# Kernel optimization log

Measured on AMD Instinct MI355X. Metric: run time of the kernel, lower is better.

The kernel has to match this reference:

```python
import jax, jax.numpy as jnp
import numpy as np

EPS = 1e-12

def l2norm(x):
    return x / jnp.maximum(jnp.linalg.norm(x, axis=-1, keepdims=True), EPS)

def setup_inputs() -> dict:
    key = jax.random.key(0)
    ks = jax.random.split(key, 10)
    B, N, Din, D, P, C = 2, 32768, 768, 512, 16, 2
    return {
        "x_s": jax.random.normal(ks[0], (B, N, Din), jnp.float32),
        "coord_s": jax.random.uniform(ks[1], (B, N, 2), jnp.float32),
        "x_l": jax.random.normal(ks[2], (B, N, Din), jnp.float32),
        "coord_l": jax.random.uniform(ks[3], (B, N, 2), jnp.float32),
        "W_proj": jax.random.normal(ks[4], (Din, D), jnp.float32) / np.sqrt(Din),
        "b_proj": jax.random.normal(ks[5], (D,), jnp.float32) * 0.01,
        "prototypes": jax.random.normal(ks[6], (P, D), jnp.float32),
        "text_low": l2norm(jax.random.normal(ks[7], (C, D), jnp.float32)),
        "text_high": l2norm(jax.random.normal(ks[8], (C, D), jnp.float32)),
        "label": jax.random.randint(ks[9], (B,), 0, C, jnp.int64),
    }

def forward_project(x, W, b):
    # Linear projection to hidden size, then L2 normalize (matches visual.forward_project + F.normalize)
    return l2norm(jnp.einsum('bni,id->bnd', x, W) + b)

def attention_pool(feats, prototypes):
    # feats: [B,N,D], prototypes: [P,D]
    D = feats.shape[-1]
    p = l2norm(prototypes)
    scores = jnp.einsum('bnd,pd->bpn', feats, p) / jnp.sqrt(jnp.asarray(D, feats.dtype))
    w = jax.nn.softmax(scores, axis=-1)                  # [B,P,N]
    attended = jnp.einsum('bpn,bnd->bpd', w, feats)       # [B,P,D]
    return l2norm(attended.mean(axis=1))                  # [B,D]

def reference(x_s, coord_s, x_l, coord_l, W_proj, b_proj, prototypes, text_low, text_high, label):
    x_s_proj = forward_project(x_s, W_proj, b_proj)
    x_l_proj = forward_project(x_l, W_proj, b_proj)
    feat_low = attention_pool(x_s_proj, prototypes)
    feat_high = attention_pool(x_l_proj, prototypes)
    logits = feat_low @ text_low.T + feat_high @ text_high.T   # [B,C]
    logp = jax.nn.log_softmax(logits, axis=-1)
    loss = -jnp.mean(jnp.take_along_axis(logp, label[:, None], axis=1))
    Y_prob = jax.nn.softmax(logits, axis=1)
    Y_hat = jnp.argmax(Y_prob, axis=1)
    return Y_prob, Y_hat, loss
```

## Files before the change

### kernel.cpp

```cpp
#include <hip/hip_runtime.h>
#include <math.h>

#define BB   2
#define NN   32768
#define DIN  768
#define DD   512
#define PP   16
#define MTOT (BB*NN)
#define MALL (2*MTOT)
#define NCHUNK 128
#define CHUNK  (NN/NCHUNK)
#define SCALE_INV_SQRT_D 0.04419417382415922f

typedef unsigned short u16;
typedef __attribute__((ext_vector_type(8))) short bf16x8;
typedef __attribute__((ext_vector_type(4))) float f32x4;

#define MFMA(a,b,c) __builtin_amdgcn_mfma_f32_16x16x32_bf16((a),(b),(c),0,0,0)

__device__ __forceinline__ unsigned pack2bf(float a, float b) {
  union { float f; unsigned u; } x{a}, y{b};
  unsigned ra = (x.u + 0x7FFFu + ((x.u >> 16) & 1u)) >> 16;
  unsigned rb = (y.u + 0x7FFFu + ((y.u >> 16) & 1u)) >> 16;
  return ra | (rb << 16);
}
__device__ __forceinline__ u16 f2bf(float a) {
  union { float f; unsigned u; } x{a};
  return (u16)((x.u + 0x7FFFu + ((x.u >> 16) & 1u)) >> 16);
}
__device__ __forceinline__ float bf2f(u16 u) {
  union { unsigned u; float f; } x; x.u = ((unsigned)u) << 16; return x.f;
}

__device__ __forceinline__ float block_reduce_sum_256(float v, float* sred) {
  #pragma unroll
  for (int off = 32; off; off >>= 1) v += __shfl_down(v, off);
  const int lane = threadIdx.x & 63, w = threadIdx.x >> 6;
  if (lane == 0) sred[w] = v;
  __syncthreads();
  float r = sred[0] + sred[1] + sred[2] + sred[3];
  __syncthreads();
  return r;
}

__global__ __launch_bounds__(64) void pre_kernel(
    const float* __restrict__ W, const float* __restrict__ prot,
    uint4* __restrict__ Bf, uint4* __restrict__ pnb) {
  const int bid = blockIdx.x;
  const int lane = threadIdx.x;
  if (bid < 768) {
    const int nf = bid / 24, ks = bid % 24;
    const int n = nf*16 + (lane & 15);
    const int kb = ks*32 + (lane >> 4)*8;
    unsigned r0 = pack2bf(W[(size_t)(kb+0)*DD + n], W[(size_t)(kb+1)*DD + n]);
    unsigned r1 = pack2bf(W[(size_t)(kb+2)*DD + n], W[(size_t)(kb+3)*DD + n]);
    unsigned r2 = pack2bf(W[(size_t)(kb+4)*DD + n], W[(size_t)(kb+5)*DD + n]);
    unsigned r3 = pack2bf(W[(size_t)(kb+6)*DD + n], W[(size_t)(kb+7)*DD + n]);
    Bf[(size_t)bid*64 + lane] = make_uint4(r0, r1, r2, r3);
    return;
  }
  const int ks = bid - 768;
  const int p = lane & 15, seg = lane >> 4;
  float ssq = 0.f;
  for (int d = seg*128; d < seg*128 + 128; d += 4) {
    float4 v = *(const float4*)&prot[p*DD + d];
    ssq += v.x*v.x + v.y*v.y + v.z*v.z + v.w*v.w;
  }
  ssq += __shfl_xor(ssq, 16);
  ssq += __shfl_xor(ssq, 32);
  const float rnp = 1.f / fmaxf(sqrtf(ssq), 1e-12f);
  const int kb = ks*32 + seg*8;
  float v[8];
  #pragma unroll
  for (int j = 0; j < 8; ++j) v[j] = prot[p*DD + kb + j] * rnp;
  pnb[ks*64 + lane] = make_uint4(pack2bf(v[0],v[1]), pack2bf(v[2],v[3]),
                                 pack2bf(v[4],v[5]), pack2bf(v[6],v[7]));
}

__global__ __launch_bounds__(512, 4) void gemm_kernel(
    const float* __restrict__ Xs, const float* __restrict__ Xl,
    const uint4* __restrict__ Bf, const float* __restrict__ bias,
    u16* __restrict__ proj, float* __restrict__ rnormb) {
  __shared__ __align__(16) unsigned char lds[73728];
  const int t = threadIdx.x, lane = t & 63, wn = t >> 6;
  const int cl = lane & 15, cg = lane >> 4;
  const int m0g = blockIdx.x * 64;
  const float* Xb = (m0g < MTOT) ? Xs : Xl;
  const int m0l = m0g & (MTOT - 1);
  const int r = t >> 3, c4 = t & 7;
  const float* gA = Xb + (size_t)(m0l + r) * DIN + c4 * 4;
  const int awoff = (r >> 4)*1024 + ((r & 15) + 16*(c4 >> 1))*16 + (c4 & 1)*8;

  f32x4 acc[4][4] = {};

#define STAGE_B(ktx, buf) \
  { _Pragma("unroll") \
    for (int q_ = 0; q_ < 4; ++q_) { \
      const int c_ = q_*8 + wn; \
      const uint4* src_ = Bf + ((size_t)(c_*24 + (ktx)))*64 + lane; \
      __builtin_amdgcn_global_load_lds( \
          (const __attribute__((address_space(1))) void*)src_, \
          (__attribute__((address_space(3))) void*)(lds + 8192 + (buf)*32768 + c_*1024 + lane*16), \
          16, 0, 0); \
    } }

  {
    STAGE_B(0, 0);
    float4 va = *(const float4*)gA;
    *(uint2*)(lds + awoff) = make_uint2(pack2bf(va.x, va.y), pack2bf(va.z, va.w));
  }
  __syncthreads();
  for (int kt = 0; kt < 24; ++kt) {
    const int cur = kt & 1;
    float4 va;
    if (kt < 23) {
      STAGE_B(kt + 1, cur ^ 1);
      va = *(const float4*)(gA + (kt + 1) * 32);
    }
    bf16x8 af[4], bfr[4];
    #pragma unroll
    for (int m = 0; m < 4; ++m)
      af[m] = *(const bf16x8*)(lds + cur*4096 + m*1024 + lane*16);
    #pragma unroll
    for (int j = 0; j < 4; ++j)
      bfr[j] = *(const bf16x8*)(lds + 8192 + cur*32768 + (wn*4 + j)*1024 + lane*16);
    #pragma unroll
    for (int j = 0; j < 4; ++j)
      #pragma unroll
      for (int m = 0; m < 4; ++m)
        acc[m][j] = MFMA(af[m], bfr[j], acc[m][j]);
    if (kt < 23) {
      *(uint2*)(lds + (cur^1)*4096 + awoff) =
          make_uint2(pack2bf(va.x, va.y), pack2bf(va.z, va.w));
    }
    __syncthreads();
  }
#undef STAGE_B
  float* ssqred = (float*)lds;
  float bv[4];
  #pragma unroll
  for (int j = 0; j < 4; ++j) bv[j] = bias[wn*64 + j*16 + cl];
  #pragma unroll
  for (int m = 0; m < 4; ++m) {
    #pragma unroll
    for (int rr = 0; rr < 4; ++rr) {
      const int rowl = m*16 + cg*4 + rr;
      u16* pr = proj + (size_t)(m0g + rowl) * DD + wn*64 + cl;
      float sq = 0.f;
      #pragma unroll
      for (int j = 0; j < 4; ++j) {
        float val = acc[m][j][rr] + bv[j];
        pr[j*16] = f2bf(val);
        sq += val * val;
      }
      sq += __shfl_xor(sq, 1); sq += __shfl_xor(sq, 2);
      sq += __shfl_xor(sq, 4); sq += __shfl_xor(sq, 8);
      if (cl == 0) ssqred[rowl*8 + wn] = sq;
    }
  }
  __syncthreads();
  if (t < 64) {
    float ss = 0.f;
    #pragma unroll
    for (int w = 0; w < 8; ++w) ss += ssqred[t*8 + w];
    rnormb[m0g + t] = 1.f / fmaxf(sqrtf(ss), 1e-12f);
  }
}

__global__ __launch_bounds__(256) void scores_kernel(
    const u16* __restrict__ proj, const uint4* __restrict__ pnb,
    const float* __restrict__ rnormb, u16* __restrict__ wbufe,
    float* __restrict__ espart) {
  __shared__ float esp[4][16];
  __shared__ u16 sbuf[128][18];
  const int t = threadIdx.x, lane = t & 63, wave = t >> 6;
  const int cl = lane & 15, cg = lane >> 4;
  bf16x8 pf[16];
  #pragma unroll
  for (int ks = 0; ks < 16; ++ks) pf[ks] = *(const bf16x8*)(pnb + ks*64 + lane);
  const int row0b = blockIdx.x * 128;
  float esum = 0.f;
  #pragma unroll
  for (int rg = 0; rg < 2; ++rg) {
    const int row0 = row0b + wave*32 + rg*16;
    f32x4 sacc = {0.f, 0.f, 0.f, 0.f};
    #pragma unroll
    for (int ks = 0; ks < 16; ++ks) {
      bf16x8 af = *(const bf16x8*)(proj + (size_t)(row0 + cl)*DD + ks*32 + cg*8);
      sacc = MFMA(af, pf[ks], sacc);
    }
    #pragma unroll
    for (int rr = 0; rr < 4; ++rr) {
      const int grow = row0 + cg*4 + rr;
      const float sc = sacc[rr] * rnormb[grow] * SCALE_INV_SQRT_D;
      const float e = expf(sc);
      esum += e;
      sbuf[wave*32 + rg*16 + cg*4 + rr][cl] = f2bf(e);
    }
  }
  esum += __shfl_xor(esum, 16);
  esum += __shfl_xor(esum, 32);
  if (lane < 16) esp[wave][lane] = esum;
  __syncthreads();
  if (t < 16)
    espart[(size_t)blockIdx.x * PP + t] = esp[0][t] + esp[1][t] + esp[2][t] + esp[3][t];
  {
    const int p = t >> 4, i8 = (t & 15) * 8;
    const int sbp = row0b >> 15, nb0 = row0b & (NN - 1);
    u16 tmp[8];
    #pragma unroll
    for (int k = 0; k < 8; ++k) tmp[k] = sbuf[i8 + k][p];
    *(uint4*)&wbufe[(size_t)(sbp*PP + p) * NN + nb0 + i8] = *(const uint4*)tmp;
  }
}

__global__ __launch_bounds__(256) void isum_kernel(const float* __restrict__ espart,
                                                   float* __restrict__ iSrow) {
  __shared__ float sred[4];
  const int bid = blockIdx.x, sbp = bid >> 4, p = bid & 15;
  const int t = threadIdx.x;
  float s = espart[(size_t)(sbp*256 + t)*PP + p];
  s = block_reduce_sum_256(s, sred);
  if (t == 0) iSrow[bid] = 1.f / s;
}

__global__ __launch_bounds__(256) void attended_kernel(
    const u16* __restrict__ proj, const u16* __restrict__ wbufe,
    const float* __restrict__ rnormb, const float* __restrict__ iSrow,
    float* __restrict__ part) {
  __shared__ float wl[CHUNK];
  __shared__ float iSl[PP];
  const int sb = blockIdx.y, cid = blockIdx.x, t = threadIdx.x;
  const int nbase = cid * CHUNK;
  if (t < PP) iSl[t] = iSrow[sb*PP + t];
  __syncthreads();
  if (t < CHUNK) {
    const int n = nbase + t;
    float s = 0.f;
    #pragma unroll
    for (int p = 0; p < PP; ++p)
      s += bf2f(wbufe[(size_t)(sb*PP + p)*NN + n]) * iSl[p];
    wl[t] = s * rnormb[sb*NN + n] * (1.f / PP);
  }
  __syncthreads();
  float a0 = 0.f, a1 = 0.f;
  const u16* pb = proj + ((size_t)sb * NN + nbase) * DD + 2*t;
  #pragma unroll 8
  for (int n = 0; n < CHUNK; ++n) {
    unsigned uu = *(const unsigned*)(pb + (size_t)n * DD);
    float w = wl[n];
    a0 += w * bf2f((u16)uu);
    a1 += w * bf2f((u16)(uu >> 16));
  }
  *(float2*)&part[((size_t)(sb*NCHUNK + cid))*DD + 2*t] = make_float2(a0, a1);
}

__global__ __launch_bounds__(256) void featred_kernel(
    const float* __restrict__ part, float* __restrict__ fraw) {
  __shared__ float red[2][128];
  const int sb = blockIdx.y, d0 = blockIdx.x * 128, t = threadIdx.x;
  const int dl = t & 127, half = t >> 7;
  float s = 0.f;
  for (int c = half*64; c < half*64 + 64; ++c)
    s += part[((size_t)(sb*NCHUNK + c))*DD + d0 + dl];
  red[half][dl] = s;
  __syncthreads();
  if (t < 128) fraw[sb*DD + d0 + t] = red[0][t] + red[1][t];
}

__global__ __launch_bounds__(256) void final_kernel(
    const float* __restrict__ fraw, const float* __restrict__ textL,
    const float* __restrict__ textH, const int* __restrict__ label,
    float* __restrict__ out) {
  __shared__ float sred[4];
  const int t = threadIdx.x;
  const float* frawL = fraw;
  const float* frawH = fraw + 2*DD;
  float invL[2], invH[2];
  #pragma unroll
  for (int b = 0; b < 2; ++b) {
    float v = 0.f;
    for (int d = t; d < DD; d += 256) { float x = frawL[b*DD + d]; v += x*x; }
    float ss = block_reduce_sum_256(v, sred);
    invL[b] = 1.f / fmaxf(sqrtf(ss), 1e-12f);
    v = 0.f;
    for (int d = t; d < DD; d += 256) { float x = frawH[b*DD + d]; v += x*x; }
    ss = block_reduce_sum_256(v, sred);
    invH[b] = 1.f / fmaxf(sqrtf(ss), 1e-12f);
  }
  float lg[2][2];
  #pragma unroll
  for (int b = 0; b < 2; ++b)
    #pragma unroll
    for (int c = 0; c < 2; ++c) {
      float v = 0.f;
      for (int d = t; d < DD; d += 256)
        v += frawL[b*DD + d] * invL[b] * textL[c*DD + d]
           + frawH[b*DD + d] * invH[b] * textH[c*DD + d];
      lg[b][c] = block_reduce_sum_256(v, sred);
    }
  if (t == 0) {
    float loss = 0.f;
    #pragma unroll
    for (int b = 0; b < 2; ++b) {
      const float m  = fmaxf(lg[b][0], lg[b][1]);
      const float lse = m + logf(expf(lg[b][0]-m) + expf(lg[b][1]-m));
      out[b*2+0] = expf(lg[b][0]-lse); out[b*2+1] = expf(lg[b][1]-lse);
      out[4+b] = (lg[b][1] > lg[b][0]) ? 1.f : 0.f;
      loss += -(lg[b][label[b]] - lse);
    }
    out[6] = loss * 0.5f;
  }
}

extern "C" void kernel_launch(void* const* d_in, const int* in_sizes, int n_in,
                              void* d_out, int out_size, void* d_ws, size_t ws_size,
                              hipStream_t stream) {
  (void)in_sizes; (void)n_in; (void)out_size; (void)ws_size;
  const float* x_s  = (const float*)d_in[0];
  const float* x_l  = (const float*)d_in[2];
  const float* Wp   = (const float*)d_in[4];
  const float* bp   = (const float*)d_in[5];
  const float* prot = (const float*)d_in[6];
  const float* tL   = (const float*)d_in[7];
  const float* tH   = (const float*)d_in[8];
  const int*   label= (const int*)d_in[9];
  float* out = (float*)d_out;

  unsigned char* w8 = (unsigned char*)d_ws;
  u16*   proj   = (u16*)  (w8);
  u16*   wbufe  = (u16*)  (w8 + 134217728);
  float* part   = (float*)(w8 + 138412032);
  float* rnormb = (float*)(w8 + 139460608);
  float* espart = (float*)(w8 + 139984896);
  float* iSrow  = (float*)(w8 + 140050432);
  uint4* Bf     = (uint4*)(w8 + 140051456);
  uint4* pnb    = (uint4*)(w8 + 140837888);
  float* fraw   = (float*)(w8 + 140854272);

  pre_kernel<<<784, 64, 0, stream>>>(Wp, prot, Bf, pnb);
  gemm_kernel<<<MALL/64, 512, 0, stream>>>(x_s, x_l, Bf, bp, proj, rnormb);
  scores_kernel<<<MALL/128, 256, 0, stream>>>(proj, pnb, rnormb, wbufe, espart);
  isum_kernel<<<64, 256, 0, stream>>>(espart, iSrow);
  attended_kernel<<<dim3(NCHUNK, 4), 256, 0, stream>>>(proj, wbufe, rnormb, iSrow, part);
  featred_kernel<<<dim3(4, 4), 256, 0, stream>>>(part, fraw);
  final_kernel<<<1, 256, 0, stream>>>(fraw, tL, tH, label, out);
}
```

Baseline: 250.1 us.

## Retile projection GEMM to 256x256 blocks with split-N partial norms

The projection GEMM moves from 64-row blocks covering all 512 columns to 256x256 tiles, each wave computing 128x64. Each K step now covers 64 instead of 32, and block IDs are swizzled so the two N-halves of the same rows run close together. The intent is to raise arithmetic intensity and cut repeated B-matrix traffic per output. Because a block now sees only half of each row, it writes partial sums of squares, and the scores kernel combines them and computes the reciprocal norm. The cost is a larger LDS footprint (128KB) and more accumulators, which limits occupancy to roughly one or two blocks per CU.

```diff
diff --git a/kernel.cpp b/kernel.cpp
--- a/kernel.cpp
+++ b/kernel.cpp
@@ -77,100 +77,114 @@
                                  pack2bf(v[4],v[5]), pack2bf(v[6],v[7]));
 }
 
-__global__ __launch_bounds__(512, 4) void gemm_kernel(
+__global__ __launch_bounds__(512, 2) void gemm_kernel(
     const float* __restrict__ Xs, const float* __restrict__ Xl,
     const uint4* __restrict__ Bf, const float* __restrict__ bias,
-    u16* __restrict__ proj, float* __restrict__ rnormb) {
-  __shared__ __align__(16) unsigned char lds[73728];
-  const int t = threadIdx.x, lane = t & 63, wn = t >> 6;
+    u16* __restrict__ proj, float* __restrict__ ssqp2) {
+  __shared__ __align__(16) unsigned char lds[131072];
+  const int t = threadIdx.x, lane = t & 63, wid = t >> 6;
+  const int wm = wid >> 2, wn = wid & 3;
   const int cl = lane & 15, cg = lane >> 4;
-  const int m0g = blockIdx.x * 64;
+  const int id = blockIdx.x;
+  const int swz = (id & 7) * 128 + (id >> 3);
+  const int mb = swz >> 1, nb = swz & 1;
+  const int m0g = mb * 256;
   const float* Xb = (m0g < MTOT) ? Xs : Xl;
   const int m0l = m0g & (MTOT - 1);
-  const int r = t >> 3, c4 = t & 7;
-  const float* gA = Xb + (size_t)(m0l + r) * DIN + c4 * 4;
-  const int awoff = (r >> 4)*1024 + ((r & 15) + 16*(c4 >> 1))*16 + (c4 & 1)*8;
-
-  f32x4 acc[4][4] = {};
+  const int r = t >> 1, kh1 = t & 1;
+  const float* gA = Xb + (size_t)(m0l + r) * DIN + kh1 * 32;
+  const int abase = ((((r >> 4) * 2 + kh1) << 10) + ((r & 15) << 4));
+
+  f32x4 acc[8][4] = {};
 
 #define STAGE_B(ktx, buf) \
   { _Pragma("unroll") \
     for (int q_ = 0; q_ < 4; ++q_) { \
-      const int c_ = q_*8 + wn; \
-      const uint4* src_ = Bf + ((size_t)(c_*24 + (ktx)))*64 + lane; \
+      const int c_ = q_*8 + wid; \
+      const uint4* src_ = Bf + ((size_t)((nb*16 + (c_>>1))*24 + (ktx)*2 + (c_&1)))*64 + lane; \
       __builtin_amdgcn_global_load_lds( \
           (const __attribute__((address_space(1))) void*)src_, \
-          (__attribute__((address_space(3))) void*)(lds + 8192 + (buf)*32768 + c_*1024 + lane*16), \
+          (__attribute__((address_space(3))) void*)(lds + 65536 + (buf)*32768 + c_*1024 + lane*16), \
           16, 0, 0); \
     } }
+#define PACK_A(dstbuf, va) \
+  { _Pragma("unroll") \
+    for (int p4_ = 0; p4_ < 4; ++p4_) { \
+      *(uint4*)(lds + (dstbuf)*32768 + abase + p4_*256) = make_uint4( \
+          pack2bf(va[2*p4_].x,   va[2*p4_].y), pack2bf(va[2*p4_].z,   va[2*p4_].w), \
+          pack2bf(va[2*p4_+1].x, va[2*p4_+1].y), pack2bf(va[2*p4_+1].z, va[2*p4_+1].w)); \
+    } }
 
   {
+    float4 va[8];
+    #pragma unroll
+    for (int q = 0; q < 8; ++q) va[q] = *(const float4*)(gA + q*4);
+    PACK_A(0, va);
     STAGE_B(0, 0);
-    float4 va = *(const float4*)gA;
-    *(uint2*)(lds + awoff) = make_uint2(pack2bf(va.x, va.y), pack2bf(va.z, va.w));
-  }
-  __syncthreads();
-  for (int kt = 0; kt < 24; ++kt) {
+    __syncthreads();
+  }
+  for (int kt = 0; kt < 12; ++kt) {
     const int cur = kt & 1;
-    float4 va;
-    if (kt < 23) {
+    float4 va[8];
+    if (kt < 11) {
+      #pragma unroll
+      for (int q = 0; q < 8; ++q) va[q] = *(const float4*)(gA + (kt+1)*64 + q*4);
       STAGE_B(kt + 1, cur ^ 1);
-      va = *(const float4*)(gA + (kt + 1) * 32);
-    }
-    bf16x8 af[4], bfr[4];
-    #pragma unroll
-    for (int m = 0; m < 4; ++m)
-      af[m] = *(const bf16x8*)(lds + cur*4096 + m*1024 + lane*16);
-    #pragma unroll
-    for (int j = 0; j < 4; ++j)
-      bfr[j] = *(const bf16x8*)(lds + 8192 + cur*32768 + (wn*4 + j)*1024 + lane*16);
-    #pragma unroll
-    for (int j = 0; j < 4; ++j)
-      #pragma unroll
-      for (int m = 0; m < 4; ++m)
-        acc[m][j] = MFMA(af[m], bfr[j], acc[m][j]);
-    if (kt < 23) {
-      *(uint2*)(lds + (cur^1)*4096 + awoff) =
-          make_uint2(pack2bf(va.x, va.y), pack2bf(va.z, va.w));
-    }
+    }
+    const int Ab = cur*32768, Bb = 65536 + cur*32768;
+    #pragma unroll
+    for (int ksl = 0; ksl < 2; ++ksl) {
+      bf16x8 bfr[4], af[8];
+      #pragma unroll
+      for (int j = 0; j < 4; ++j)
+        bfr[j] = *(const bf16x8*)(lds + Bb + ((((wn*4 + j)*2 + ksl)) << 10) + lane*16);
+      #pragma unroll
+      for (int i = 0; i < 8; ++i)
+        af[i] = *(const bf16x8*)(lds + Ab + ((((wm*8 + i)*2 + ksl)) << 10) + lane*16);
+      #pragma unroll
+      for (int i = 0; i < 8; ++i)
+        #pragma unroll
+        for (int j = 0; j < 4; ++j)
+          acc[i][j] = MFMA(af[i], bfr[j], acc[i][j]);
+    }
+    if (kt < 11) PACK_A(cur ^ 1, va);
     __syncthreads();
   }
 #undef STAGE_B
+#undef PACK_A
   float* ssqred = (float*)lds;
   float bv[4];
   #pragma unroll
-  for (int j = 0; j < 4; ++j) bv[j] = bias[wn*64 + j*16 + cl];
-  #pragma unroll
-  for (int m = 0; m < 4; ++m) {
+  for (int j = 0; j < 4; ++j) bv[j] = bias[nb*256 + wn*64 + j*16 + cl];
+  #pragma unroll
+  for (int i = 0; i < 8; ++i) {
     #pragma unroll
     for (int rr = 0; rr < 4; ++rr) {
-      const int rowl = m*16 + cg*4 + rr;
-      u16* pr = proj + (size_t)(m0g + rowl) * DD + wn*64 + cl;
+      const int rowl = wm*128 + i*16 + cg*4 + rr;
+      u16* pr = proj + (size_t)(m0g + rowl) * DD + nb*256 + wn*64 + cl;
       float sq = 0.f;
       #pragma unroll
       for (int j = 0; j < 4; ++j) {
-        float val = acc[m][j][rr] + bv[j];
+        float val = acc[i][j][rr] + bv[j];
         pr[j*16] = f2bf(val);
         sq += val * val;
       }
       sq += __shfl_xor(sq, 1); sq += __shfl_xor(sq, 2);
       sq += __shfl_xor(sq, 4); sq += __shfl_xor(sq, 8);
-      if (cl == 0) ssqred[rowl*8 + wn] = sq;
-    }
-  }
-  __syncthreads();
-  if (t < 64) {
-    float ss = 0.f;
-    #pragma unroll
-    for (int w = 0; w < 8; ++w) ss += ssqred[t*8 + w];
-    rnormb[m0g + t] = 1.f / fmaxf(sqrtf(ss), 1e-12f);
+      if (cl == 0) ssqred[rowl*4 + wn] = sq;
+    }
+  }
+  __syncthreads();
+  if (t < 256) {
+    float ss = ssqred[t*4+0] + ssqred[t*4+1] + ssqred[t*4+2] + ssqred[t*4+3];
+    ssqp2[(size_t)(m0g + t) * 2 + nb] = ss;
   }
 }
 
 __global__ __launch_bounds__(256) void scores_kernel(
     const u16* __restrict__ proj, const uint4* __restrict__ pnb,
-    const float* __restrict__ rnormb, u16* __restrict__ wbufe,
-    float* __restrict__ espart) {
+    const float* __restrict__ ssqp2, float* __restrict__ rnormb,
+    u16* __restrict__ wbufe, float* __restrict__ espart) {
   __shared__ float esp[4][16];
   __shared__ u16 sbuf[128][18];
   const int t = threadIdx.x, lane = t & 63, wave = t >> 6;
@@ -192,7 +206,10 @@
     #pragma unroll
     for (int rr = 0; rr < 4; ++rr) {
       const int grow = row0 + cg*4 + rr;
-      const float sc = sacc[rr] * rnormb[grow] * SCALE_INV_SQRT_D;
+      const float2 sp = *(const float2*)&ssqp2[(size_t)grow * 2];
+      const float rn = 1.f / fmaxf(sqrtf(sp.x + sp.y), 1e-12f);
+      if (cl == 0) rnormb[grow] = rn;
+      const float sc = sacc[rr] * rn * SCALE_INV_SQRT_D;
       const float e = expf(sc);
       esum += e;
       sbuf[wave*32 + rg*16 + cg*4 + rr][cl] = f2bf(e);
@@ -332,15 +349,16 @@
   u16*   wbufe  = (u16*)  (w8 + 134217728);
   float* part   = (float*)(w8 + 138412032);
   float* rnormb = (float*)(w8 + 139460608);
-  float* espart = (float*)(w8 + 139984896);
-  float* iSrow  = (float*)(w8 + 140050432);
-  uint4* Bf     = (uint4*)(w8 + 140051456);
-  uint4* pnb    = (uint4*)(w8 + 140837888);
-  float* fraw   = (float*)(w8 + 140854272);
+  float* ssqp2  = (float*)(w8 + 139984896);
+  float* espart = (float*)(w8 + 141033472);
+  float* iSrow  = (float*)(w8 + 141099008);
+  uint4* Bf     = (uint4*)(w8 + 141100032);
+  uint4* pnb    = (uint4*)(w8 + 141886464);
+  float* fraw   = (float*)(w8 + 141902848);
 
   pre_kernel<<<784, 64, 0, stream>>>(Wp, prot, Bf, pnb);
-  gemm_kernel<<<MALL/64, 512, 0, stream>>>(x_s, x_l, Bf, bp, proj, rnormb);
-  scores_kernel<<<MALL/128, 256, 0, stream>>>(proj, pnb, rnormb, wbufe, espart);
+  gemm_kernel<<<MALL/256*2, 512, 0, stream>>>(x_s, x_l, Bf, bp, proj, ssqp2);
+  scores_kernel<<<MALL/128, 256, 0, stream>>>(proj, pnb, ssqp2, rnormb, wbufe, espart);
   isum_kernel<<<64, 256, 0, stream>>>(espart, iSrow);
   attended_kernel<<<dim3(NCHUNK, 4), 256, 0, stream>>>(proj, wbufe, rnormb, iSrow, part);
   featred_kernel<<<dim3(4, 4), 256, 0, stream>>>(part, fraw);
```

New measurement: 303.5 us. +21.4%, slower.

## Enlarge projection GEMM tile to 128 rows with K-step 64 and swizzled A LDS

Applied to the files above, without the earlier changes.

The projection GEMM now uses 1024-thread blocks covering 128 rows by all 512 output columns, arranged as a 2x8 grid of waves, with a K step of 64 instead of 32. Each staged weight tile is reused across twice as many rows, roughly halving the weight traffic from L2 per output row, and the number of K iterations and barriers drops. A-tile LDS writes and reads use an XOR swizzle to avoid bank conflicts. In exchange, the A tile is single-buffered with an extra barrier per iteration, and the 144KB LDS footprint limits each CU to one block.

```diff
diff --git a/kernel.cpp b/kernel.cpp
--- a/kernel.cpp
+++ b/kernel.cpp
@@ -77,63 +77,75 @@
                                  pack2bf(v[4],v[5]), pack2bf(v[6],v[7]));
 }
 
-__global__ __launch_bounds__(512, 4) void gemm_kernel(
+__global__ __launch_bounds__(1024, 4) void gemm_kernel(
     const float* __restrict__ Xs, const float* __restrict__ Xl,
     const uint4* __restrict__ Bf, const float* __restrict__ bias,
     u16* __restrict__ proj, float* __restrict__ rnormb) {
-  __shared__ __align__(16) unsigned char lds[73728];
-  const int t = threadIdx.x, lane = t & 63, wn = t >> 6;
+  __shared__ __align__(16) unsigned char lds[147456];
+  const int t = threadIdx.x, lane = t & 63, wid = t >> 6;
+  const int wm = wid >> 3, wn = wid & 7;
   const int cl = lane & 15, cg = lane >> 4;
-  const int m0g = blockIdx.x * 64;
+  const int m0g = blockIdx.x * 128;
   const float* Xb = (m0g < MTOT) ? Xs : Xl;
   const int m0l = m0g & (MTOT - 1);
-  const int r = t >> 3, c4 = t & 7;
-  const float* gA = Xb + (size_t)(m0l + r) * DIN + c4 * 4;
-  const int awoff = (r >> 4)*1024 + ((r & 15) + 16*(c4 >> 1))*16 + (c4 & 1)*8;
+  const int r = t >> 3, k8g = (t & 7) * 8;
+  const float* gA = Xb + (size_t)(m0l + r) * DIN + k8g;
+  const int aksl = k8g >> 5, acg = (k8g >> 3) & 3;
+  const int awoff = ((r >> 4) * 2 + aksl) * 1024 + acg * 256
+                  + (((r & 15) ^ ((acg << 1) | aksl)) << 4);
 
   f32x4 acc[4][4] = {};
 
 #define STAGE_B(ktx, buf) \
   { _Pragma("unroll") \
     for (int q_ = 0; q_ < 4; ++q_) { \
-      const int c_ = q_*8 + wn; \
-      const uint4* src_ = Bf + ((size_t)(c_*24 + (ktx)))*64 + lane; \
+      const int c_ = q_*16 + wid; \
+      const uint4* src_ = Bf + ((size_t)((c_>>1)*24 + (ktx)*2 + (c_&1)))*64 + lane; \
       __builtin_amdgcn_global_load_lds( \
           (const __attribute__((address_space(1))) void*)src_, \
-          (__attribute__((address_space(3))) void*)(lds + 8192 + (buf)*32768 + c_*1024 + lane*16), \
+          (__attribute__((address_space(3))) void*)(lds + 16384 + (buf)*65536 + c_*1024 + lane*16), \
           16, 0, 0); \
     } }
 
   {
     STAGE_B(0, 0);
-    float4 va = *(const float4*)gA;
-    *(uint2*)(lds + awoff) = make_uint2(pack2bf(va.x, va.y), pack2bf(va.z, va.w));
-  }
-  __syncthreads();
-  for (int kt = 0; kt < 24; ++kt) {
-    const int cur = kt & 1;
-    float4 va;
-    if (kt < 23) {
-      STAGE_B(kt + 1, cur ^ 1);
-      va = *(const float4*)(gA + (kt + 1) * 32);
-    }
-    bf16x8 af[4], bfr[4];
-    #pragma unroll
-    for (int m = 0; m < 4; ++m)
-      af[m] = *(const bf16x8*)(lds + cur*4096 + m*1024 + lane*16);
-    #pragma unroll
-    for (int j = 0; j < 4; ++j)
-      bfr[j] = *(const bf16x8*)(lds + 8192 + cur*32768 + (wn*4 + j)*1024 + lane*16);
-    #pragma unroll
-    for (int j = 0; j < 4; ++j)
+    float4 a0 = *(const float4*)gA;
+    float4 a1 = *(const float4*)(gA + 4);
+    *(uint4*)(lds + awoff) = make_uint4(pack2bf(a0.x,a0.y), pack2bf(a0.z,a0.w),
+                                        pack2bf(a1.x,a1.y), pack2bf(a1.z,a1.w));
+    __syncthreads();
+  }
+  for (int kt = 0; kt < 12; ++kt) {
+    const int bcur = kt & 1;
+    float4 a0, a1;
+    if (kt < 11) {
+      STAGE_B(kt + 1, bcur ^ 1);
+      a0 = *(const float4*)(gA + (kt + 1) * 64);
+      a1 = *(const float4*)(gA + (kt + 1) * 64 + 4);
+    }
+    #pragma unroll
+    for (int ksl = 0; ksl < 2; ++ksl) {
+      bf16x8 af[4], bfr[4];
       #pragma unroll
-      for (int m = 0; m < 4; ++m)
-        acc[m][j] = MFMA(af[m], bfr[j], acc[m][j]);
-    if (kt < 23) {
-      *(uint2*)(lds + (cur^1)*4096 + awoff) =
-          make_uint2(pack2bf(va.x, va.y), pack2bf(va.z, va.w));
+      for (int i = 0; i < 4; ++i)
+        af[i] = *(const bf16x8*)(lds + ((wm*4 + i)*2 + ksl)*1024 + cg*256
+                                     + ((cl ^ ((cg << 1) | ksl)) << 4));
+      #pragma unroll
+      for (int j = 0; j < 4; ++j)
+        bfr[j] = *(const bf16x8*)(lds + 16384 + bcur*65536
+                                      + ((wn*4 + j)*2 + ksl)*1024 + lane*16);
+      #pragma unroll
+      for (int i = 0; i < 4; ++i)
+        #pragma unroll
+        for (int j = 0; j < 4; ++j)
+          acc[i][j] = MFMA(af[i], bfr[j], acc[i][j]);
     }
     __syncthreads();
+    if (kt < 11) {
+      *(uint4*)(lds + awoff) = make_uint4(pack2bf(a0.x,a0.y), pack2bf(a0.z,a0.w),
+                                          pack2bf(a1.x,a1.y), pack2bf(a1.z,a1.w));
+      __syncthreads();
+    }
   }
 #undef STAGE_B
   float* ssqred = (float*)lds;
@@ -141,15 +153,15 @@
   #pragma unroll
   for (int j = 0; j < 4; ++j) bv[j] = bias[wn*64 + j*16 + cl];
   #pragma unroll
-  for (int m = 0; m < 4; ++m) {
+  for (int i = 0; i < 4; ++i) {
     #pragma unroll
     for (int rr = 0; rr < 4; ++rr) {
-      const int rowl = m*16 + cg*4 + rr;
+      const int rowl = wm*64 + i*16 + cg*4 + rr;
       u16* pr = proj + (size_t)(m0g + rowl) * DD + wn*64 + cl;
       float sq = 0.f;
       #pragma unroll
       for (int j = 0; j < 4; ++j) {
-        float val = acc[m][j][rr] + bv[j];
+        float val = acc[i][j][rr] + bv[j];
         pr[j*16] = f2bf(val);
         sq += val * val;
       }
@@ -159,7 +171,7 @@
     }
   }
   __syncthreads();
-  if (t < 64) {
+  if (t < 128) {
     float ss = 0.f;
     #pragma unroll
     for (int w = 0; w < 8; ++w) ss += ssqred[t*8 + w];
@@ -339,7 +351,7 @@
   float* fraw   = (float*)(w8 + 140854272);
 
   pre_kernel<<<784, 64, 0, stream>>>(Wp, prot, Bf, pnb);
-  gemm_kernel<<<MALL/64, 512, 0, stream>>>(x_s, x_l, Bf, bp, proj, rnormb);
+  gemm_kernel<<<MALL/128, 1024, 0, stream>>>(x_s, x_l, Bf, bp, proj, rnormb);
   scores_kernel<<<MALL/128, 256, 0, stream>>>(proj, pnb, rnormb, wbufe, espart);
   isum_kernel<<<64, 256, 0, stream>>>(espart, iSrow);
   attended_kernel<<<dim3(NCHUNK, 4), 256, 0, stream>>>(proj, wbufe, rnormb, iSrow, part);
```

Result: faster. 221.3 us (-11.5%).
